# Kernel optimization log

Measured on AMD Instinct MI355X. Metric: run time of the kernel, lower is better.

Reference implementation:

```python
import jax, jax.numpy as jnp
import numpy as np

V, E, H, C = 50000, 256, 512, 2   # vocab, embed_dim, hidden_dim, num_classes
B, L = 64, 512                    # batch, seq_len
PAD_IDX = 0


def _xavier(key, shape):
    fan_out, fan_in = shape
    lim = np.sqrt(6.0 / (fan_in + fan_out)).astype(np.float32)
    return jax.random.uniform(key, shape, jnp.float32, -lim, lim)


def setup_inputs() -> dict:
    key = jax.random.key(0)
    ks = jax.random.split(key, 8)
    embed = jax.random.normal(ks[0], (V, E), jnp.float32) * 0.02
    embed = embed.at[PAD_IDX].set(0.0)  # nn.Embedding padding_idx row is zero
    inp = E + H
    Wf = _xavier(ks[1], (H, inp)); bf = jnp.zeros((H,), jnp.float32)
    Wi = _xavier(ks[2], (H, inp)); bi = jnp.zeros((H,), jnp.float32)
    Wc = _xavier(ks[3], (H, inp)); bc = jnp.zeros((H,), jnp.float32)
    Wo = _xavier(ks[4], (H, inp)); bo = jnp.zeros((H,), jnp.float32)
    Wfc = _xavier(ks[5], (C, H)); bfc = jnp.zeros((C,), jnp.float32)
    x = jax.random.randint(ks[6], (B, L), 0, V)
    mask = jnp.ones((B, L), dtype=bool)
    return dict(x=x, mask=mask, embed=embed, Wf=Wf, bf=bf, Wi=Wi, bi=bi,
                Wc=Wc, bc=bc, Wo=Wo, bo=bo, Wfc=Wfc, bfc=bfc)


def reference(x, mask, embed, Wf, bf, Wi, bi, Wc, bc, Wo, bo, Wfc, bfc):
    emb = embed[x]                      # [B,L,E]  (dropout=0 -> identity)
    m = mask.astype(jnp.float32)        # [B,L]

    def step(carry, inp):
        h, c = carry                    # [B,H] each
        x_t, m_t = inp                  # [B,E], [B]
        comb = jnp.concatenate([x_t, h], axis=1)       # [B,E+H]
        f = jax.nn.sigmoid(comb @ Wf.T + bf)
        i = jax.nn.sigmoid(comb @ Wi.T + bi)
        c_tilde = jnp.tanh(comb @ Wc.T + bc)
        c = f * c + i * c_tilde
        o = jax.nn.sigmoid(comb @ Wo.T + bo)
        h_new = o * jnp.tanh(c)
        mt = m_t[:, None]
        h = h_new * mt + h * (1.0 - mt)
        # original: c = c*m + c*(1-m)  -> identity, replicated as no-op
        return (h, c), h

    h0 = jnp.zeros((x.shape[0], Wf.shape[0]), jnp.float32)
    (_, _), hs = jax.lax.scan(step, (h0, h0), (emb.transpose(1, 0, 2), m.T))
    all_hidden = hs.transpose(1, 0, 2)                 # [B,L,H]

    # pooling == 'mean'
    denom = jnp.clip(m.sum(axis=1, keepdims=True), 1e-9)
    rep = (all_hidden * m[:, :, None]).sum(axis=1) / denom   # [B,H]
    logits = rep @ Wfc.T + bfc                               # [B,C]
    return logits, rep
```

## Files before the change

### kernel.cpp

```cpp
#include <hip/hip_runtime.h>

constexpr int B = 64, L = 512, E = 256, H = 512;
constexpr int ROWS = 4 * H;
constexpr int K    = E + H;
constexpr int K4   = K / 4;

constexpr size_t OFF_WT4   = 0;
constexpr size_t SZ_WT4    = (size_t)K4 * ROWS * 4;
constexpr size_t OFF_BI    = OFF_WT4 + SZ_WT4;
constexpr size_t SZ_BI     = ROWS;
constexpr size_t OFF_H2    = OFF_BI + SZ_BI;
constexpr size_t SZ_H2     = (size_t)2 * B * H * 2;
constexpr size_t OFF_REP   = OFF_H2 + SZ_H2;
constexpr size_t SZ_REP    = (size_t)B * H;
constexpr size_t WS_FLOATS = OFF_REP + SZ_REP;

__global__ __launch_bounds__(256) void prep_weights(
    const float* __restrict__ Wf, const float* __restrict__ Wi,
    const float* __restrict__ Wc, const float* __restrict__ Wo,
    const float* __restrict__ bf, const float* __restrict__ bi,
    const float* __restrict__ bc, const float* __restrict__ bo,
    float* __restrict__ ws)
{
    float* WT4 = ws + OFF_WT4;
    float* bI  = ws + OFF_BI;
    int idx = blockIdx.x * 256 + threadIdx.x;
    const float* Ws[4] = {Wf, Wi, Wc, Wo};
    #pragma unroll
    for (int j = 0; j < 6; ++j) {
        int item = idx + j * 65536;
        int k4   = item >> 11;
        int row  = item & 2047;
        int unit = row >> 2, gate = row & 3;
        const float* W = Ws[gate];
        float4 v = *(const float4*)(W + (size_t)unit * K + (size_t)k4 * 4);
        *(float4*)(WT4 + ((size_t)k4 * ROWS + row) * 4) = v;
    }
    if (idx < ROWS) {
        int unit = idx >> 2, gate = idx & 3;
        const float* bs[4] = {bf, bi, bc, bo};
        bI[idx] = bs[gate][unit];
    }
    ((unsigned long long*)(ws + OFF_H2))[idx] = 0ull;
}

__global__ __launch_bounds__(512, 2) void lstm_persist(
    float* __restrict__ ws,
    const int* __restrict__ x, const int* __restrict__ mask,
    const float* __restrict__ embed)
{
    __shared__ float emb_lds[2][8][E];
    __shared__ float h_lds[8 * H];
    __shared__ float part2_lds[8 * 16 * 64];

    const int bid = blockIdx.x;
    const int rg  = bid >> 3, sg = bid & 7;
    const int tid = threadIdx.x;
    const int w   = tid >> 6, l = tid & 63;
    const int q   = l >> 4, rl = l & 15;
    const int m   = w * 4 + q;
    const int seq_base = sg * 8;
    const int gate = l & 3, qlane = l >> 2;

    const float4* WT4 = (const float4*)(ws + OFF_WT4);
    const float*  bI  = ws + OFF_BI;
    unsigned long long* h2 = (unsigned long long*)(ws + OFF_H2);
    float* repg = ws + OFF_REP;

    float4 wreg[24];
    {
        const int rowA = rg * 64 + rl * 4;
        #pragma unroll
        for (int jj = 0; jj < 2; ++jj)
            #pragma unroll
            for (int r = 0; r < 4; ++r)
                wreg[r * 2 + jj] = WT4[(size_t)(w * 8 + q + 4 * jj) * ROWS + rowA + r];
        #pragma unroll
        for (int jj = 0; jj < 4; ++jj)
            #pragma unroll
            for (int r = 0; r < 4; ++r)
                wreg[8 + r * 4 + jj] = WT4[(size_t)(64 + w * 16 + q + 4 * jj) * ROWS + rowA + r];
    }
    const float breg = bI[rg * 64 + l];

    float c0 = 0.f, h0 = 0.f, r0 = 0.f;

    const int sl = tid >> 6, col = (tid & 63) * 4;

    {
        int tok = x[(size_t)(seq_base + sl) * L + 0];
        *(float4*)&emb_lds[0][sl][col] = *(const float4*)(embed + (size_t)tok * E + col);
        #pragma unroll
        for (int i = 0; i < 8; ++i) h_lds[tid + i * 512] = 0.f;
    }
    __syncthreads();

    for (int t = 0; t < L; ++t) {
        const int cur = t & 1, nxt = cur ^ 1;
        const unsigned long long* c2c = h2 + (size_t)cur * B * H + (size_t)seq_base * H;
        unsigned long long*       c2n = h2 + (size_t)nxt * B * H + (size_t)seq_base * H;

        float4 e0;
        const bool pf = (t + 1) < L;
        if (pf) {
            int tok = x[(size_t)(seq_base + sl) * L + (t + 1)];
            e0 = *(const float4*)(embed + (size_t)tok * E + col);
        }

        unsigned long long hv[8];
        if (t > 0) {
            #pragma unroll
            for (int i = 0; i < 4; ++i) {
                hv[2 * i]     = __hip_atomic_load(&c2c[i * 1024 + tid * 2],
                                    __ATOMIC_RELAXED, __HIP_MEMORY_SCOPE_AGENT);
                hv[2 * i + 1] = __hip_atomic_load(&c2c[i * 1024 + tid * 2 + 1],
                                    __ATOMIC_RELAXED, __HIP_MEMORY_SCOPE_AGENT);
            }
        }

        float acc[4][8];
        #pragma unroll
        for (int r = 0; r < 4; ++r)
            #pragma unroll
            for (int s8 = 0; s8 < 8; ++s8) acc[r][s8] = 0.f;
        #pragma unroll
        for (int jj = 0; jj < 2; ++jj) {
            const int off = (w * 8 + q + 4 * jj) * 4;
            #pragma unroll
            for (int s8 = 0; s8 < 8; ++s8) {
                float4 c4 = *(const float4*)&emb_lds[cur][s8][off];
                #pragma unroll
                for (int r = 0; r < 4; ++r) {
                    float4 wv = wreg[r * 2 + jj];
                    acc[r][s8] = fmaf(wv.x, c4.x, acc[r][s8]);
                    acc[r][s8] = fmaf(wv.y, c4.y, acc[r][s8]);
                    acc[r][s8] = fmaf(wv.z, c4.z, acc[r][s8]);
                    acc[r][s8] = fmaf(wv.w, c4.w, acc[r][s8]);
                }
            }
        }

        if (t > 0) {
            const unsigned int want = (unsigned int)(t + 1);
            int guard = 0;
            for (;;) {
                bool ok = true;
                #pragma unroll
                for (int i = 0; i < 8; ++i)
                    ok &= ((unsigned int)(hv[i] >> 32) == want);
                if (__all(ok) || ++guard > (1 << 20)) break;
                __builtin_amdgcn_s_sleep(2);
                #pragma unroll
                for (int i = 0; i < 4; ++i) {
                    hv[2 * i]     = __hip_atomic_load(&c2c[i * 1024 + tid * 2],
                                        __ATOMIC_RELAXED, __HIP_MEMORY_SCOPE_AGENT);
                    hv[2 * i + 1] = __hip_atomic_load(&c2c[i * 1024 + tid * 2 + 1],
                                        __ATOMIC_RELAXED, __HIP_MEMORY_SCOPE_AGENT);
                }
            }
            #pragma unroll
            for (int i = 0; i < 4; ++i)
                *(float2*)&h_lds[i * 1024 + tid * 2] = make_float2(
                    __uint_as_float((unsigned int)hv[2 * i]),
                    __uint_as_float((unsigned int)hv[2 * i + 1]));
        }

        if (pf) *(float4*)&emb_lds[nxt][sl][col] = e0;
        __syncthreads();

        #pragma unroll
        for (int jj = 0; jj < 4; ++jj) {
            const int off = (w * 16 + q + 4 * jj) * 4;
            #pragma unroll
            for (int s8 = 0; s8 < 8; ++s8) {
                float4 c4 = *(const float4*)&h_lds[s8 * 512 + off];
                #pragma unroll
                for (int r = 0; r < 4; ++r) {
                    float4 wv = wreg[8 + r * 4 + jj];
                    acc[r][s8] = fmaf(wv.x, c4.x, acc[r][s8]);
                    acc[r][s8] = fmaf(wv.y, c4.y, acc[r][s8]);
                    acc[r][s8] = fmaf(wv.z, c4.z, acc[r][s8]);
                    acc[r][s8] = fmaf(wv.w, c4.w, acc[r][s8]);
                }
            }
        }

        if (w < 4) {
            #pragma unroll
            for (int s8 = 0; s8 < 8; ++s8)
                *(float4*)&part2_lds[(s8 * 16 + m) * 64 + rl * 4] =
                    make_float4(acc[0][s8], acc[1][s8], acc[2][s8], acc[3][s8]);
        }
        __syncthreads();
        if (w >= 4) {
            #pragma unroll
            for (int s8 = 0; s8 < 8; ++s8) {
                float4* p = (float4*)&part2_lds[(s8 * 16 + (m - 16)) * 64 + rl * 4];
                float4 o = *p;
                o.x += acc[0][s8]; o.y += acc[1][s8];
                o.z += acc[2][s8]; o.w += acc[3][s8];
                *p = o;
            }
        }
        __syncthreads();

        {
            float a = breg;
            #pragma unroll
            for (int mm = 0; mm < 16; ++mm)
                a += part2_lds[(w * 16 + mm) * 64 + l];
            float act = (gate == 2) ? tanhf(a) : 1.f / (1.f + expf(-a));
            int ab = __float_as_int(act);
            float fg = __int_as_float(__builtin_amdgcn_mov_dpp(ab, 0x00, 0xF, 0xF, true));
            float ig = __int_as_float(__builtin_amdgcn_mov_dpp(ab, 0x55, 0xF, 0xF, true));
            float cg = __int_as_float(__builtin_amdgcn_mov_dpp(ab, 0xAA, 0xF, 0xF, true));
            float og = __int_as_float(__builtin_amdgcn_mov_dpp(ab, 0xFF, 0xF, 0xF, true));
            if (gate == 0) {
                c0 = fg * c0 + ig * cg;
                float hn = og * tanhf(c0);
                int seq = seq_base + w;
                float mk = (mask[(size_t)seq * L + t] != 0) ? 1.f : 0.f;
                float h = hn * mk + h0 * (1.f - mk);
                h0 = h;
                unsigned long long p64 = (((unsigned long long)(unsigned int)(t + 2)) << 32)
                                       | (unsigned long long)__float_as_uint(h);
                __hip_atomic_store(&c2n[(size_t)w * H + rg * 16 + qlane],
                                   p64, __ATOMIC_RELAXED, __HIP_MEMORY_SCOPE_AGENT);
                r0 += h * mk;
            }
        }
    }

    if (gate == 0)
        repg[(size_t)(seq_base + w) * H + rg * 16 + qlane] = r0;
}

__global__ __launch_bounds__(256) void lstm_final(
    const float* __restrict__ ws,
    const int* __restrict__ mask,
    const float* __restrict__ Wfc, const float* __restrict__ bfc,
    float* __restrict__ out)
{
    __shared__ float sred[256];
    __shared__ float srep[H];
    int s = blockIdx.x, tid = threadIdx.x;

    float dsum = 0.f;
    for (int i = tid; i < L; i += 256) dsum += (mask[(size_t)s * L + i] != 0) ? 1.f : 0.f;
    sred[tid] = dsum; __syncthreads();
    for (int off = 128; off > 0; off >>= 1) {
        if (tid < off) sred[tid] += sred[tid + off];
        __syncthreads();
    }
    float denom = fmaxf(sred[0], 1e-9f);
    __syncthreads();

    const float* repa = ws + OFF_REP + (size_t)s * H;
    for (int i = tid; i < H; i += 256) {
        float r = repa[i] / denom;
        srep[i] = r;
        out[128 + (size_t)s * H + i] = r;
    }
    __syncthreads();

    for (int c = 0; c < 2; ++c) {
        float d = 0.f;
        for (int i = tid; i < H; i += 256) d += srep[i] * Wfc[(size_t)c * H + i];
        sred[tid] = d; __syncthreads();
        for (int off = 128; off > 0; off >>= 1) {
            if (tid < off) sred[tid] += sred[tid + off];
            __syncthreads();
        }
        if (tid == 0) out[(size_t)s * 2 + c] = sred[0] + bfc[c];
        __syncthreads();
    }
}

extern "C" void kernel_launch(void* const* d_in, const int* in_sizes, int n_in,
                              void* d_out, int out_size, void* d_ws, size_t ws_size,
                              hipStream_t stream)
{
    const int*   x     = (const int*)d_in[0];
    const int*   mask  = (const int*)d_in[1];
    const float* embed = (const float*)d_in[2];
    const float* Wf = (const float*)d_in[3];  const float* bf = (const float*)d_in[4];
    const float* Wi = (const float*)d_in[5];  const float* bi = (const float*)d_in[6];
    const float* Wc = (const float*)d_in[7];  const float* bc = (const float*)d_in[8];
    const float* Wo = (const float*)d_in[9];  const float* bo = (const float*)d_in[10];
    const float* Wfc = (const float*)d_in[11]; const float* bfc = (const float*)d_in[12];
    float* out = (float*)d_out;
    float* ws  = (float*)d_ws;

    if (ws_size < WS_FLOATS * sizeof(float)) {
        return;
    }

    prep_weights<<<256, 256, 0, stream>>>(Wf, Wi, Wc, Wo, bf, bi, bc, bo, ws);
    lstm_persist<<<256, 512, 0, stream>>>(ws, x, mask, embed);
    lstm_final<<<64, 256, 0, stream>>>(ws, mask, Wfc, bfc, out);
}
```

Measured before the change: 1.972 ms.

## Double threads per block in persistent LSTM, halving per-thread K slice

Grows the persistent LSTM blocks from 512 to 1024 threads, so each thread holds half as many weight registers and covers half the K dimension. Partial sums from paired lanes are combined with a DPP row-shift add before the LDS reduction, and only the first 8 waves run the gate activation and state update. The aim is shorter serial FMA chains per step on the latency-bound recurrence, paid for with an extra DPP reduction, more threads per barrier and tighter register limits at 1024 threads.

```diff
diff --git a/kernel.cpp b/kernel.cpp
--- a/kernel.cpp
+++ b/kernel.cpp
@@ -44,7 +44,7 @@
     ((unsigned long long*)(ws + OFF_H2))[idx] = 0ull;
 }
 
-__global__ __launch_bounds__(512, 2) void lstm_persist(
+__global__ __launch_bounds__(1024, 4) void lstm_persist(
     float* __restrict__ ws,
     const int* __restrict__ x, const int* __restrict__ mask,
     const float* __restrict__ embed)
@@ -57,8 +57,9 @@
     const int rg  = bid >> 3, sg = bid & 7;
     const int tid = threadIdx.x;
     const int w   = tid >> 6, l = tid & 63;
-    const int q   = l >> 4, rl = l & 15;
-    const int m   = w * 4 + q;
+    const int q   = (l >> 3) & 3;
+    const int rl4 = (l & 7) | ((l >> 5) << 3);
+    const int qhalf = (l >> 4) & 1;
     const int seq_base = sg * 8;
     const int gate = l & 3, qlane = l >> 2;
 
@@ -67,31 +68,29 @@
     unsigned long long* h2 = (unsigned long long*)(ws + OFF_H2);
     float* repg = ws + OFF_REP;
 
-    float4 wreg[24];
+    float4 wreg[12];
     {
-        const int rowA = rg * 64 + rl * 4;
+        const int rowA = rg * 64 + rl4 * 4;
+        #pragma unroll
+        for (int r = 0; r < 4; ++r)
+            wreg[r] = WT4[(size_t)(w * 4 + q) * ROWS + rowA + r];
         #pragma unroll
         for (int jj = 0; jj < 2; ++jj)
             #pragma unroll
             for (int r = 0; r < 4; ++r)
-                wreg[r * 2 + jj] = WT4[(size_t)(w * 8 + q + 4 * jj) * ROWS + rowA + r];
-        #pragma unroll
-        for (int jj = 0; jj < 4; ++jj)
-            #pragma unroll
-            for (int r = 0; r < 4; ++r)
-                wreg[8 + r * 4 + jj] = WT4[(size_t)(64 + w * 16 + q + 4 * jj) * ROWS + rowA + r];
+                wreg[4 + r * 2 + jj] = WT4[(size_t)(64 + w * 8 + q + 4 * jj) * ROWS + rowA + r];
     }
     const float breg = bI[rg * 64 + l];
 
     float c0 = 0.f, h0 = 0.f, r0 = 0.f;
 
-    const int sl = tid >> 6, col = (tid & 63) * 4;
+    const int sl = tid >> 7, col2 = (tid & 127) * 2;
 
     {
         int tok = x[(size_t)(seq_base + sl) * L + 0];
-        *(float4*)&emb_lds[0][sl][col] = *(const float4*)(embed + (size_t)tok * E + col);
-        #pragma unroll
-        for (int i = 0; i < 8; ++i) h_lds[tid + i * 512] = 0.f;
+        *(float2*)&emb_lds[0][sl][col2] = *(const float2*)(embed + (size_t)tok * E + col2);
+        #pragma unroll
+        for (int i = 0; i < 4; ++i) h_lds[tid + i * 1024] = 0.f;
     }
     __syncthreads();
 
@@ -100,20 +99,20 @@
         const unsigned long long* c2c = h2 + (size_t)cur * B * H + (size_t)seq_base * H;
         unsigned long long*       c2n = h2 + (size_t)nxt * B * H + (size_t)seq_base * H;
 
-        float4 e0;
+        float2 e0;
         const bool pf = (t + 1) < L;
         if (pf) {
             int tok = x[(size_t)(seq_base + sl) * L + (t + 1)];
-            e0 = *(const float4*)(embed + (size_t)tok * E + col);
-        }
-
-        unsigned long long hv[8];
+            e0 = *(const float2*)(embed + (size_t)tok * E + col2);
+        }
+
+        unsigned long long hv[4];
         if (t > 0) {
             #pragma unroll
-            for (int i = 0; i < 4; ++i) {
-                hv[2 * i]     = __hip_atomic_load(&c2c[i * 1024 + tid * 2],
+            for (int i = 0; i < 2; ++i) {
+                hv[2 * i]     = __hip_atomic_load(&c2c[i * 2048 + tid * 2],
                                     __ATOMIC_RELAXED, __HIP_MEMORY_SCOPE_AGENT);
-                hv[2 * i + 1] = __hip_atomic_load(&c2c[i * 1024 + tid * 2 + 1],
+                hv[2 * i + 1] = __hip_atomic_load(&c2c[i * 2048 + tid * 2 + 1],
                                     __ATOMIC_RELAXED, __HIP_MEMORY_SCOPE_AGENT);
             }
         }
@@ -123,15 +122,14 @@
         for (int r = 0; r < 4; ++r)
             #pragma unroll
             for (int s8 = 0; s8 < 8; ++s8) acc[r][s8] = 0.f;
-        #pragma unroll
-        for (int jj = 0; jj < 2; ++jj) {
-            const int off = (w * 8 + q + 4 * jj) * 4;
+        {
+            const int off = (w * 4 + q) * 4;
             #pragma unroll
             for (int s8 = 0; s8 < 8; ++s8) {
                 float4 c4 = *(const float4*)&emb_lds[cur][s8][off];
                 #pragma unroll
                 for (int r = 0; r < 4; ++r) {
-                    float4 wv = wreg[r * 2 + jj];
+                    float4 wv = wreg[r];
                     acc[r][s8] = fmaf(wv.x, c4.x, acc[r][s8]);
                     acc[r][s8] = fmaf(wv.y, c4.y, acc[r][s8]);
                     acc[r][s8] = fmaf(wv.z, c4.z, acc[r][s8]);
@@ -146,37 +144,37 @@
             for (;;) {
                 bool ok = true;
                 #pragma unroll
-                for (int i = 0; i < 8; ++i)
+                for (int i = 0; i < 4; ++i)
                     ok &= ((unsigned int)(hv[i] >> 32) == want);
                 if (__all(ok) || ++guard > (1 << 20)) break;
                 __builtin_amdgcn_s_sleep(2);
                 #pragma unroll
-                for (int i = 0; i < 4; ++i) {
-                    hv[2 * i]     = __hip_atomic_load(&c2c[i * 1024 + tid * 2],
+                for (int i = 0; i < 2; ++i) {
+                    hv[2 * i]     = __hip_atomic_load(&c2c[i * 2048 + tid * 2],
                                         __ATOMIC_RELAXED, __HIP_MEMORY_SCOPE_AGENT);
-                    hv[2 * i + 1] = __hip_atomic_load(&c2c[i * 1024 + tid * 2 + 1],
+                    hv[2 * i + 1] = __hip_atomic_load(&c2c[i * 2048 + tid * 2 + 1],
                                         __ATOMIC_RELAXED, __HIP_MEMORY_SCOPE_AGENT);
                 }
             }
             #pragma unroll
-            for (int i = 0; i < 4; ++i)
-                *(float2*)&h_lds[i * 1024 + tid * 2] = make_float2(
+            for (int i = 0; i < 2; ++i)
+                *(float2*)&h_lds[i * 2048 + tid * 2] = make_float2(
                     __uint_as_float((unsigned int)hv[2 * i]),
                     __uint_as_float((unsigned int)hv[2 * i + 1]));
         }
 
-        if (pf) *(float4*)&emb_lds[nxt][sl][col] = e0;
-        __syncthreads();
-
-        #pragma unroll
-        for (int jj = 0; jj < 4; ++jj) {
-            const int off = (w * 16 + q + 4 * jj) * 4;
+        if (pf) *(float2*)&emb_lds[nxt][sl][col2] = e0;
+        __syncthreads();
+
+        #pragma unroll
+        for (int jj = 0; jj < 2; ++jj) {
+            const int off = (w * 8 + q + 4 * jj) * 4;
             #pragma unroll
             for (int s8 = 0; s8 < 8; ++s8) {
                 float4 c4 = *(const float4*)&h_lds[s8 * 512 + off];
                 #pragma unroll
                 for (int r = 0; r < 4; ++r) {
-                    float4 wv = wreg[8 + r * 4 + jj];
+                    float4 wv = wreg[4 + r * 2 + jj];
                     acc[r][s8] = fmaf(wv.x, c4.x, acc[r][s8]);
                     acc[r][s8] = fmaf(wv.y, c4.y, acc[r][s8]);
                     acc[r][s8] = fmaf(wv.z, c4.z, acc[r][s8]);
@@ -185,17 +183,29 @@
             }
         }
 
-        if (w < 4) {
+        #pragma unroll
+        for (int r = 0; r < 4; ++r)
+            #pragma unroll
+            for (int s8 = 0; s8 < 8; ++s8) {
+                int a_ = __float_as_int(acc[r][s8]);
+                float o = __int_as_float(
+                    __builtin_amdgcn_mov_dpp(a_, 0x128, 0xF, 0xF, true));
+                acc[r][s8] += o;
+            }
+
+        if (w < 8 && (q & 1) == 0) {
+            const int s = w * 2 + qhalf;
             #pragma unroll
             for (int s8 = 0; s8 < 8; ++s8)
-                *(float4*)&part2_lds[(s8 * 16 + m) * 64 + rl * 4] =
+                *(float4*)&part2_lds[(s8 * 16 + s) * 64 + rl4 * 4] =
                     make_float4(acc[0][s8], acc[1][s8], acc[2][s8], acc[3][s8]);
         }
         __syncthreads();
-        if (w >= 4) {
+        if (w >= 8 && (q & 1) == 0) {
+            const int s = (w - 8) * 2 + qhalf;
             #pragma unroll
             for (int s8 = 0; s8 < 8; ++s8) {
-                float4* p = (float4*)&part2_lds[(s8 * 16 + (m - 16)) * 64 + rl * 4];
+                float4* p = (float4*)&part2_lds[(s8 * 16 + s) * 64 + rl4 * 4];
                 float4 o = *p;
                 o.x += acc[0][s8]; o.y += acc[1][s8];
                 o.z += acc[2][s8]; o.w += acc[3][s8];
@@ -204,7 +214,7 @@
         }
         __syncthreads();
 
-        {
+        if (w < 8) {
             float a = breg;
             #pragma unroll
             for (int mm = 0; mm < 16; ++mm)
@@ -231,7 +241,7 @@
         }
     }
 
-    if (gate == 0)
+    if (w < 8 && gate == 0)
         repg[(size_t)(seq_base + w) * H + rg * 16 + qlane] = r0;
 }
 
@@ -296,6 +306,6 @@
     }
 
     prep_weights<<<256, 256, 0, stream>>>(Wf, Wi, Wc, Wo, bf, bi, bc, bo, ws);
-    lstm_persist<<<256, 512, 0, stream>>>(ws, x, mask, embed);
+    lstm_persist<<<256, 1024, 0, stream>>>(ws, x, mask, embed);
     lstm_final<<<64, 256, 0, stream>>>(ws, mask, Wfc, bfc, out);
 }
```

After: 4.445 ms. 125% more time.
